# Kernel optimization log

Measured on AMD Instinct MI355X. Metric: run time of the kernel, lower is better.

The kernel has to match this reference:

```python
import jax, jax.numpy as jnp
import numpy as np

N_HEADS = 16
D_HEAD = 64  # embed_dim // n_heads = 1024 // 16


def setup_inputs() -> dict:
    key = jax.random.key(0)
    ks = jax.random.split(key, 8)
    B, S, E = 2, 2048, 1024
    return {
        "k_in": jax.random.normal(ks[0], (B, S, E), jnp.float32),
        "q_in": jax.random.normal(ks[1], (B, S, E), jnp.float32),
        "v_in": jax.random.normal(ks[2], (B, S, E), jnp.float32),
        "Wq": jax.random.normal(ks[3], (D_HEAD, D_HEAD), jnp.float32) / np.sqrt(D_HEAD),
        "Wk": jax.random.normal(ks[4], (D_HEAD, D_HEAD), jnp.float32) / np.sqrt(D_HEAD),
        "Wv": jax.random.normal(ks[5], (D_HEAD, D_HEAD), jnp.float32) / np.sqrt(D_HEAD),
        "Wo": jax.random.normal(ks[6], (E, E), jnp.float32) / np.sqrt(E),
        "bo": jnp.zeros((E,), jnp.float32),
    }


def reference(k_in, q_in, v_in, Wq, Wk, Wv, Wo, bo):
    B, Sq, E = q_in.shape
    Sk = k_in.shape[1]
    H, Dh = N_HEADS, D_HEAD
    # split heads: [B, S, H, Dh]
    q = q_in.reshape(B, Sq, H, Dh)
    k = k_in.reshape(B, Sk, H, Dh)
    v = v_in.reshape(B, Sk, H, Dh)
    # per-head linear projections (nn.Linear: x @ W.T), then [B, H, S, Dh]
    q = jnp.einsum("bshd,ed->bhse", q, Wq)
    k = jnp.einsum("bshd,ed->bhse", k, Wk)
    v = jnp.einsum("bshd,ed->bhse", v, Wv)
    # scaled dot-product attention
    scores = jnp.einsum("bhqd,bhkd->bhqk", q, k) / jnp.sqrt(jnp.asarray(Dh, q.dtype))
    attn = jax.nn.softmax(scores, axis=-1)
    ctx = jnp.einsum("bhqk,bhkd->bqhd", attn, v)  # [B, Sq, H, Dh]
    concat = ctx.reshape(B, Sq, H * Dh)
    return concat @ Wo.T + bo
```

## Files before the change

kernel.cpp:

```cpp
#include <hip/hip_runtime.h>
#include <hip/hip_fp16.h>

typedef _Float16 f16;
typedef _Float16 f16x8 __attribute__((ext_vector_type(8)));
typedef _Float16 f16x4v __attribute__((ext_vector_type(4)));
typedef float f32x4 __attribute__((ext_vector_type(4)));

#define B_ 2
#define S_ 2048
#define E_ 1024
#define H_ 16
#define DH_ 64

__device__ __forceinline__ f32x4 mfma16(f16x8 a, f16x8 b, f32x4 c) {
    return __builtin_amdgcn_mfma_f32_16x16x32_f16(a, b, c, 0, 0, 0);
}

__device__ __forceinline__ f16x8 cvt8(const float* p) {
    float4 v0 = *(const float4*)p;
    float4 v1 = *(const float4*)(p + 4);
    f16x8 r;
    r[0] = (f16)v0.x; r[1] = (f16)v0.y; r[2] = (f16)v0.z; r[3] = (f16)v0.w;
    r[4] = (f16)v1.x; r[5] = (f16)v1.y; r[6] = (f16)v1.z; r[7] = (f16)v1.w;
    return r;
}

__global__ __launch_bounds__(256) void proj_kernel(
    const float* __restrict__ q_in, const float* __restrict__ k_in,
    const float* __restrict__ v_in,
    const float* __restrict__ Wq, const float* __restrict__ Wk,
    const float* __restrict__ Wv,
    f16* __restrict__ Qg, f16* __restrict__ Kg, f16* __restrict__ Vt)
{
    int tid = threadIdx.x;
    int lane = tid & 63, wv = tid >> 6;
    int wid = blockIdx.x * 4 + wv;
    int proj = wid >> 12;
    int r = wid & 4095;
    int bh = r >> 7;
    int stile = r & 127;
    int sbase = stile * 16;
    int h = bh & 15;
    int b = bh >> 4;
    int c = lane & 15, g = lane >> 4;

    const float* x; const float* W;
    if (proj == 0)      { x = q_in; W = Wq; }
    else if (proj == 1) { x = k_in; W = Wk; }
    else                { x = v_in; W = Wv; }

    const float* xrow = x + (((size_t)(b * S_ + sbase + c) * H_ + h) << 6);
    f16x8 a0 = cvt8(xrow + g * 8);
    f16x8 a1 = cvt8(xrow + 32 + g * 8);

    f32x4 acc[4] = {};
#pragma unroll
    for (int nt = 0; nt < 4; ++nt) {
        const float* wrow = W + ((nt * 16 + c) << 6);
        f16x8 b0 = cvt8(wrow + g * 8);
        f16x8 b1 = cvt8(wrow + 32 + g * 8);
        acc[nt] = mfma16(a0, b0, acc[nt]);
        acc[nt] = mfma16(a1, b1, acc[nt]);
    }

    if (proj < 2) {
        f16* out = (proj == 0) ? Qg : Kg;
#pragma unroll
        for (int nt = 0; nt < 4; ++nt)
#pragma unroll
            for (int j = 0; j < 4; ++j) {
                int s = sbase + g * 4 + j;
                out[((size_t)bh * S_ + s) * DH_ + nt * 16 + c] = (f16)acc[nt][j];
            }
    } else {
#pragma unroll
        for (int nt = 0; nt < 4; ++nt) {
            f16x4v pk;
            pk[0] = (f16)acc[nt][0]; pk[1] = (f16)acc[nt][1];
            pk[2] = (f16)acc[nt][2]; pk[3] = (f16)acc[nt][3];
            *(f16x4v*)&Vt[((size_t)bh * DH_ + nt * 16 + c) * S_ + sbase + g * 4] = pk;
        }
    }
}

__global__ __launch_bounds__(256) void cvt_wo(const float* __restrict__ W,
                                              f16* __restrict__ out)
{
    int i = blockIdx.x * 256 + threadIdx.x;
    float4 v = *(const float4*)(W + (size_t)i * 4);
    f16x4v o;
    o[0] = (f16)v.x; o[1] = (f16)v.y; o[2] = (f16)v.z; o[3] = (f16)v.w;
    *(f16x4v*)(out + (size_t)i * 4) = o;
}

#define C1_ 0.18033688011112042f

__global__ __launch_bounds__(512, 4) void attn_kernel(
    const f16* __restrict__ Qg, const f16* __restrict__ Kg,
    const f16* __restrict__ Vt, f16* __restrict__ ctx)
{
    __shared__ __align__(16) f16 Kl[2][64 * 64];
    __shared__ __align__(16) f16 Vl[2][64 * 64];
    __shared__ __align__(16) f16 Pl[8][16 * 64];

    int tid = threadIdx.x, lane = tid & 63, wv = tid >> 6;
    int bx = blockIdx.x;
    int bh = bx >> 4, qt = bx & 15;
    int b = bh >> 4, h = bh & 15;
    int qbase = qt * 128 + wv * 16;
    int c = lane & 15, g = lane >> 4;
    int swz = (c & 7) << 3;

    const f16* Qh = Qg + (size_t)bh * S_ * DH_;
    const f16* Kh = Kg + (size_t)bh * S_ * DH_;
    const f16* Vh = Vt + (size_t)bh * DH_ * S_;

    int srow = tid >> 3, scc = tid & 7;
    int sdst = srow * 64 + ((scc * 8) ^ ((srow & 7) << 3));
    const f16* ksrc = Kh + (size_t)srow * DH_ + scc * 8;
    const f16* vsrc = Vh + (size_t)srow * S_ + scc * 8;

    f16x8 qf[2];
#pragma unroll
    for (int hh = 0; hh < 2; ++hh)
        qf[hh] = *(const f16x8*)(Qh + (size_t)(qbase + c) * DH_ + hh * 32 + g * 8);

    float m2 = -1e30f, lr = 0.f;
    f32x4 accO[4] = {};

    f16x8 kreg = *(const f16x8*)ksrc;
    f16x8 vreg = *(const f16x8*)vsrc;
    *(f16x8*)&Kl[0][sdst] = kreg;
    *(f16x8*)&Vl[0][sdst] = vreg;
    __syncthreads();

    int cur = 0;
#pragma unroll 1
    for (int kt = 0; kt < 32; ++kt) {
        if (kt < 31) {
            kreg = *(const f16x8*)(ksrc + (size_t)(kt + 1) * 64 * DH_);
            vreg = *(const f16x8*)(vsrc + (kt + 1) * 64);
        }

        const f16* KA = &Kl[cur][0];
        const f16* VA = &Vl[cur][0];

        f32x4 accS[4] = {};
#pragma unroll
        for (int ks = 0; ks < 4; ++ks) {
            f16x8 k0 = *(const f16x8*)&KA[(ks * 16 + c) * 64 + ((8 * g) ^ swz)];
            f16x8 k1 = *(const f16x8*)&KA[(ks * 16 + c) * 64 + ((32 + 8 * g) ^ swz)];
            accS[ks] = mfma16(k0, qf[0], accS[ks]);
            accS[ks] = mfma16(k1, qf[1], accS[ks]);
        }

        float rmax = fmaxf(fmaxf(accS[0][0], accS[0][1]),
                           fmaxf(accS[0][2], accS[0][3]));
#pragma unroll
        for (int ks = 1; ks < 4; ++ks)
#pragma unroll
            for (int j = 0; j < 4; ++j) rmax = fmaxf(rmax, accS[ks][j]);
        rmax = fmaxf(rmax, __shfl_xor(rmax, 16));
        rmax = fmaxf(rmax, __shfl_xor(rmax, 32));
        float pm2 = rmax * C1_;

        float al = 1.f;
        if (!__all(pm2 - m2 <= 8.f)) {
            float mn = fmaxf(m2, pm2);
            al = exp2f(m2 - mn);
            m2 = mn;
#pragma unroll
            for (int j = 0; j < 4; ++j) {
                float aj = __shfl(al, 4 * g + j);
#pragma unroll
                for (int nt = 0; nt < 4; ++nt) accO[nt][j] *= aj;
            }
        }

        float rs = 0.f;
        float p[4][4];
#pragma unroll
        for (int ks = 0; ks < 4; ++ks)
#pragma unroll
            for (int j = 0; j < 4; ++j) {
                float pv = exp2f(fmaf(accS[ks][j], C1_, -m2));
                p[ks][j] = pv; rs += pv;
            }
        rs += __shfl_xor(rs, 16);
        rs += __shfl_xor(rs, 32);
        lr = lr * al + rs;

#pragma unroll
        for (int ks = 0; ks < 4; ++ks) {
            f16x4v w;
            w[0] = (f16)p[ks][0]; w[1] = (f16)p[ks][1];
            w[2] = (f16)p[ks][2]; w[3] = (f16)p[ks][3];
            *(f16x4v*)&Pl[wv][c * 64 + ((16 * ks + 4 * g) ^ swz)] = w;
        }

#pragma unroll
        for (int kh = 0; kh < 2; ++kh) {
            f16x8 pa = *(const f16x8*)&Pl[wv][c * 64 + ((32 * kh + 8 * g) ^ swz)];
#pragma unroll
            for (int nt = 0; nt < 4; ++nt) {
                f16x8 vb = *(const f16x8*)&VA[(nt * 16 + c) * 64
                                              + ((32 * kh + 8 * g) ^ swz)];
                accO[nt] = mfma16(pa, vb, accO[nt]);
            }
        }

        if (kt < 31) {
            *(f16x8*)&Kl[cur ^ 1][sdst] = kreg;
            *(f16x8*)&Vl[cur ^ 1][sdst] = vreg;
            __syncthreads();
        }
        cur ^= 1;
    }

    float inv = 1.f / lr;
#pragma unroll
    for (int j = 0; j < 4; ++j) {
        float lj = __shfl(inv, 4 * g + j);
        int s = qbase + 4 * g + j;
#pragma unroll
        for (int nt = 0; nt < 4; ++nt)
            ctx[((size_t)b * S_ + s) * E_ + h * DH_ + nt * 16 + c] =
                (f16)(accO[nt][j] * lj);
    }
}

__global__ __launch_bounds__(256) void gemm_out(
    const f16* __restrict__ A,
    const f16* __restrict__ Bw,
    const float* __restrict__ bo,
    float* __restrict__ out)
{
    __shared__ __align__(16) f16 Al[2][128 * 64];
    __shared__ __align__(16) f16 Bl[2][64 * 64];

    int tid = threadIdx.x, lane = tid & 63, wv = tid >> 6;
    int mbase = blockIdx.x * 128, nbase = blockIdx.y * 64;
    int c = lane & 15, g = lane >> 4;
    int wr = wv >> 1, wc = wv & 1;
    int swz = (c & 7) << 3;

    int arow[4], adst[4]; const f16* asrc[4];
#pragma unroll
    for (int i = 0; i < 4; ++i) {
        int slot = tid + i * 256;
        arow[i] = slot >> 3;
        int cc = slot & 7;
        adst[i] = arow[i] * 64 + ((cc * 8) ^ ((arow[i] & 7) << 3));
        asrc[i] = A + (size_t)(mbase + arow[i]) * 1024 + cc * 8;
    }
    int bdst[2]; const f16* bsrc[2];
#pragma unroll
    for (int i = 0; i < 2; ++i) {
        int slot = tid + i * 256;
        int row = slot >> 3, cc = slot & 7;
        bdst[i] = row * 64 + ((cc * 8) ^ ((row & 7) << 3));
        bsrc[i] = Bw + (size_t)(nbase + row) * 1024 + cc * 8;
    }

    f32x4 acc[4][2] = {};

    f16x8 areg[4], breg[2];
#pragma unroll
    for (int i = 0; i < 4; ++i) areg[i] = *(const f16x8*)asrc[i];
#pragma unroll
    for (int i = 0; i < 2; ++i) breg[i] = *(const f16x8*)bsrc[i];
#pragma unroll
    for (int i = 0; i < 4; ++i) *(f16x8*)&Al[0][adst[i]] = areg[i];
#pragma unroll
    for (int i = 0; i < 2; ++i) *(f16x8*)&Bl[0][bdst[i]] = breg[i];
    __syncthreads();

    int cur = 0;
#pragma unroll 1
    for (int ks = 0; ks < 16; ++ks) {
        if (ks < 15) {
#pragma unroll
            for (int i = 0; i < 4; ++i)
                areg[i] = *(const f16x8*)(asrc[i] + (ks + 1) * 64);
#pragma unroll
            for (int i = 0; i < 2; ++i)
                breg[i] = *(const f16x8*)(bsrc[i] + (ks + 1) * 64);
        }

        const f16* AA = &Al[cur][0];
        const f16* BB = &Bl[cur][0];
#pragma unroll
        for (int kk = 0; kk < 2; ++kk) {
            f16x8 af[4], bf[2];
#pragma unroll
            for (int mi = 0; mi < 4; ++mi)
                af[mi] = *(const f16x8*)&AA[(wr * 64 + mi * 16 + c) * 64
                                            + ((32 * kk + 8 * g) ^ swz)];
#pragma unroll
            for (int ni = 0; ni < 2; ++ni)
                bf[ni] = *(const f16x8*)&BB[(wc * 32 + ni * 16 + c) * 64
                                            + ((32 * kk + 8 * g) ^ swz)];
#pragma unroll
            for (int mi = 0; mi < 4; ++mi)
#pragma unroll
                for (int ni = 0; ni < 2; ++ni)
                    acc[mi][ni] = mfma16(af[mi], bf[ni], acc[mi][ni]);
        }

        if (ks < 15) {
#pragma unroll
            for (int i = 0; i < 4; ++i) *(f16x8*)&Al[cur ^ 1][adst[i]] = areg[i];
#pragma unroll
            for (int i = 0; i < 2; ++i) *(f16x8*)&Bl[cur ^ 1][bdst[i]] = breg[i];
            __syncthreads();
        }
        cur ^= 1;
    }

#pragma unroll
    for (int ni = 0; ni < 2; ++ni) {
        float bias = bo[nbase + wc * 32 + ni * 16 + c];
#pragma unroll
        for (int mi = 0; mi < 4; ++mi)
#pragma unroll
            for (int j = 0; j < 4; ++j) {
                int m = mbase + wr * 64 + mi * 16 + g * 4 + j;
                out[(size_t)m * 1024 + nbase + wc * 32 + ni * 16 + c] =
                    acc[mi][ni][j] + bias;
            }
    }
}

extern "C" void kernel_launch(void* const* d_in, const int* in_sizes, int n_in,
                              void* d_out, int out_size, void* d_ws, size_t ws_size,
                              hipStream_t stream)
{
    const float* k_in = (const float*)d_in[0];
    const float* q_in = (const float*)d_in[1];
    const float* v_in = (const float*)d_in[2];
    const float* Wq   = (const float*)d_in[3];
    const float* Wk   = (const float*)d_in[4];
    const float* Wv   = (const float*)d_in[5];
    const float* Wo   = (const float*)d_in[6];
    const float* bo   = (const float*)d_in[7];
    float* out = (float*)d_out;

    char* ws = (char*)d_ws;
    f16* Qg  = (f16*)(ws);
    f16* Kg  = (f16*)(ws + (8u << 20));
    f16* Vt  = (f16*)(ws + (16u << 20));
    f16* ctx = (f16*)(ws + (24u << 20));
    f16* WoH = (f16*)(ws + (32u << 20));

    proj_kernel<<<dim3(3072), dim3(256), 0, stream>>>(q_in, k_in, v_in,
                                                      Wq, Wk, Wv, Qg, Kg, Vt);
    cvt_wo<<<dim3(1024), dim3(256), 0, stream>>>(Wo, WoH);
    attn_kernel<<<dim3(512), dim3(512), 0, stream>>>(Qg, Kg, Vt, ctx);
    gemm_out<<<dim3(32, 16), dim3(256), 0, stream>>>(ctx, WoH, bo, out);
}
```

Baseline: 121.1 us.

## Enlarge attention KV tiles, defer row-sum reduction, fuse Wo conversion into GEMM

The attention kernel now stages 128-key K/V tiles per barrier, which halves the number of loop iterations and syncs. Each tile is processed as two 64-key sub-steps. The row-sum shuffles are moved out of the loop, and the max reduction runs only when a rescale is needed. The separate Wo fp32-to-fp16 conversion kernel is removed, and gemm_out converts Wo on load, saving one launch at the cost of re-converting the weights in every block. s_setprio hints are also placed around the MFMA sections, and the doubled shared memory may lower occupancy.

```diff
diff --git a/kernel.cpp b/kernel.cpp
--- a/kernel.cpp
+++ b/kernel.cpp
@@ -83,24 +83,14 @@
     }
 }
 
-__global__ __launch_bounds__(256) void cvt_wo(const float* __restrict__ W,
-                                              f16* __restrict__ out)
-{
-    int i = blockIdx.x * 256 + threadIdx.x;
-    float4 v = *(const float4*)(W + (size_t)i * 4);
-    f16x4v o;
-    o[0] = (f16)v.x; o[1] = (f16)v.y; o[2] = (f16)v.z; o[3] = (f16)v.w;
-    *(f16x4v*)(out + (size_t)i * 4) = o;
-}
-
 #define C1_ 0.18033688011112042f
 
 __global__ __launch_bounds__(512, 4) void attn_kernel(
     const f16* __restrict__ Qg, const f16* __restrict__ Kg,
     const f16* __restrict__ Vt, f16* __restrict__ ctx)
 {
-    __shared__ __align__(16) f16 Kl[2][64 * 64];
-    __shared__ __align__(16) f16 Vl[2][64 * 64];
+    __shared__ __align__(16) f16 Kl[2][128 * 64];
+    __shared__ __align__(16) f16 Vl[2][64 * 128];
     __shared__ __align__(16) f16 Pl[8][16 * 64];
 
     int tid = threadIdx.x, lane = tid & 63, wv = tid >> 6;
@@ -115,10 +105,17 @@
     const f16* Kh = Kg + (size_t)bh * S_ * DH_;
     const f16* Vh = Vt + (size_t)bh * DH_ * S_;
 
-    int srow = tid >> 3, scc = tid & 7;
-    int sdst = srow * 64 + ((scc * 8) ^ ((srow & 7) << 3));
-    const f16* ksrc = Kh + (size_t)srow * DH_ + scc * 8;
-    const f16* vsrc = Vh + (size_t)srow * S_ + scc * 8;
+    int s0 = tid, s1 = tid + 512;
+    int kr0 = s0 >> 3, kc0 = s0 & 7, kr1 = s1 >> 3, kc1 = s1 & 7;
+    int kd0 = kr0 * 64 + ((kc0 * 8) ^ ((kr0 & 7) << 3));
+    int kd1 = kr1 * 64 + ((kc1 * 8) ^ ((kr1 & 7) << 3));
+    const f16* ksp0 = Kh + kr0 * 64 + kc0 * 8;
+    const f16* ksp1 = Kh + kr1 * 64 + kc1 * 8;
+    int vr0 = s0 >> 4, vc0 = s0 & 15, vr1 = s1 >> 4, vc1 = s1 & 15;
+    int vd0 = vr0 * 128 + ((vc0 * 8) ^ ((vr0 & 7) << 3));
+    int vd1 = vr1 * 128 + ((vc1 * 8) ^ ((vr1 & 7) << 3));
+    const f16* vsp0 = Vh + vr0 * S_ + vc0 * 8;
+    const f16* vsp1 = Vh + vr1 * S_ + vc1 * 8;
 
     f16x8 qf[2];
 #pragma unroll
@@ -128,95 +125,103 @@
     float m2 = -1e30f, lr = 0.f;
     f32x4 accO[4] = {};
 
-    f16x8 kreg = *(const f16x8*)ksrc;
-    f16x8 vreg = *(const f16x8*)vsrc;
-    *(f16x8*)&Kl[0][sdst] = kreg;
-    *(f16x8*)&Vl[0][sdst] = vreg;
+    f16x8 kreg0 = *(const f16x8*)ksp0, kreg1 = *(const f16x8*)ksp1;
+    f16x8 vreg0 = *(const f16x8*)vsp0, vreg1 = *(const f16x8*)vsp1;
+    *(f16x8*)&Kl[0][kd0] = kreg0; *(f16x8*)&Kl[0][kd1] = kreg1;
+    *(f16x8*)&Vl[0][vd0] = vreg0; *(f16x8*)&Vl[0][vd1] = vreg1;
     __syncthreads();
 
     int cur = 0;
 #pragma unroll 1
-    for (int kt = 0; kt < 32; ++kt) {
-        if (kt < 31) {
-            kreg = *(const f16x8*)(ksrc + (size_t)(kt + 1) * 64 * DH_);
-            vreg = *(const f16x8*)(vsrc + (kt + 1) * 64);
+    for (int kt = 0; kt < 16; ++kt) {
+        if (kt < 15) {
+            int ko = (kt + 1) * 128 * 64, vo = (kt + 1) * 128;
+            kreg0 = *(const f16x8*)(ksp0 + ko);
+            kreg1 = *(const f16x8*)(ksp1 + ko);
+            vreg0 = *(const f16x8*)(vsp0 + vo);
+            vreg1 = *(const f16x8*)(vsp1 + vo);
         }
 
         const f16* KA = &Kl[cur][0];
         const f16* VA = &Vl[cur][0];
 
-        f32x4 accS[4] = {};
-#pragma unroll
-        for (int ks = 0; ks < 4; ++ks) {
-            f16x8 k0 = *(const f16x8*)&KA[(ks * 16 + c) * 64 + ((8 * g) ^ swz)];
-            f16x8 k1 = *(const f16x8*)&KA[(ks * 16 + c) * 64 + ((32 + 8 * g) ^ swz)];
-            accS[ks] = mfma16(k0, qf[0], accS[ks]);
-            accS[ks] = mfma16(k1, qf[1], accS[ks]);
-        }
-
-        float rmax = fmaxf(fmaxf(accS[0][0], accS[0][1]),
-                           fmaxf(accS[0][2], accS[0][3]));
-#pragma unroll
-        for (int ks = 1; ks < 4; ++ks)
-#pragma unroll
-            for (int j = 0; j < 4; ++j) rmax = fmaxf(rmax, accS[ks][j]);
-        rmax = fmaxf(rmax, __shfl_xor(rmax, 16));
-        rmax = fmaxf(rmax, __shfl_xor(rmax, 32));
-        float pm2 = rmax * C1_;
-
-        float al = 1.f;
-        if (!__all(pm2 - m2 <= 8.f)) {
-            float mn = fmaxf(m2, pm2);
-            al = exp2f(m2 - mn);
-            m2 = mn;
-#pragma unroll
-            for (int j = 0; j < 4; ++j) {
-                float aj = __shfl(al, 4 * g + j);
-#pragma unroll
-                for (int nt = 0; nt < 4; ++nt) accO[nt][j] *= aj;
-            }
-        }
-
-        float rs = 0.f;
-        float p[4][4];
-#pragma unroll
-        for (int ks = 0; ks < 4; ++ks)
-#pragma unroll
-            for (int j = 0; j < 4; ++j) {
-                float pv = exp2f(fmaf(accS[ks][j], C1_, -m2));
-                p[ks][j] = pv; rs += pv;
-            }
-        rs += __shfl_xor(rs, 16);
-        rs += __shfl_xor(rs, 32);
-        lr = lr * al + rs;
-
-#pragma unroll
-        for (int ks = 0; ks < 4; ++ks) {
-            f16x4v w;
-            w[0] = (f16)p[ks][0]; w[1] = (f16)p[ks][1];
-            w[2] = (f16)p[ks][2]; w[3] = (f16)p[ks][3];
-            *(f16x4v*)&Pl[wv][c * 64 + ((16 * ks + 4 * g) ^ swz)] = w;
-        }
-
-#pragma unroll
-        for (int kh = 0; kh < 2; ++kh) {
-            f16x8 pa = *(const f16x8*)&Pl[wv][c * 64 + ((32 * kh + 8 * g) ^ swz)];
-#pragma unroll
-            for (int nt = 0; nt < 4; ++nt) {
-                f16x8 vb = *(const f16x8*)&VA[(nt * 16 + c) * 64
-                                              + ((32 * kh + 8 * g) ^ swz)];
-                accO[nt] = mfma16(pa, vb, accO[nt]);
-            }
-        }
-
-        if (kt < 31) {
-            *(f16x8*)&Kl[cur ^ 1][sdst] = kreg;
-            *(f16x8*)&Vl[cur ^ 1][sdst] = vreg;
+#pragma unroll
+        for (int st = 0; st < 2; ++st) {
+            f32x4 accS[4] = {};
+            __builtin_amdgcn_s_setprio(1);
+#pragma unroll
+            for (int ks = 0; ks < 4; ++ks) {
+                int krow = (st * 64 + ks * 16 + c) * 64;
+                f16x8 k0 = *(const f16x8*)&KA[krow + ((8 * g) ^ swz)];
+                f16x8 k1 = *(const f16x8*)&KA[krow + ((32 + 8 * g) ^ swz)];
+                accS[ks] = mfma16(k0, qf[0], accS[ks]);
+                accS[ks] = mfma16(k1, qf[1], accS[ks]);
+            }
+            __builtin_amdgcn_s_setprio(0);
+
+            float rmax = fmaxf(fmaxf(accS[0][0], accS[0][1]),
+                               fmaxf(accS[0][2], accS[0][3]));
+#pragma unroll
+            for (int ks = 1; ks < 4; ++ks)
+#pragma unroll
+                for (int j = 0; j < 4; ++j) rmax = fmaxf(rmax, accS[ks][j]);
+
+            if (!__all(fmaf(rmax, C1_, -m2) <= 8.f)) {
+                float mx = fmaxf(rmax, __shfl_xor(rmax, 16));
+                mx = fmaxf(mx, __shfl_xor(mx, 32));
+                float mn = fmaxf(m2, mx * C1_);
+                float al = exp2f(m2 - mn);
+                m2 = mn;
+                lr *= al;
+#pragma unroll
+                for (int j = 0; j < 4; ++j) {
+                    float aj = __shfl(al, 4 * g + j);
+#pragma unroll
+                    for (int nt = 0; nt < 4; ++nt) accO[nt][j] *= aj;
+                }
+            }
+
+            float p[4][4];
+#pragma unroll
+            for (int ks = 0; ks < 4; ++ks)
+#pragma unroll
+                for (int j = 0; j < 4; ++j) {
+                    float pv = exp2f(fmaf(accS[ks][j], C1_, -m2));
+                    p[ks][j] = pv; lr += pv;
+                }
+
+#pragma unroll
+            for (int ks = 0; ks < 4; ++ks) {
+                f16x4v w;
+                w[0] = (f16)p[ks][0]; w[1] = (f16)p[ks][1];
+                w[2] = (f16)p[ks][2]; w[3] = (f16)p[ks][3];
+                *(f16x4v*)&Pl[wv][c * 64 + ((16 * ks + 4 * g) ^ swz)] = w;
+            }
+
+            __builtin_amdgcn_s_setprio(1);
+#pragma unroll
+            for (int kh = 0; kh < 2; ++kh) {
+                f16x8 pa = *(const f16x8*)&Pl[wv][c * 64 + ((32 * kh + 8 * g) ^ swz)];
+#pragma unroll
+                for (int nt = 0; nt < 4; ++nt) {
+                    f16x8 vb = *(const f16x8*)&VA[(nt * 16 + c) * 128
+                                  + ((st * 64 + 32 * kh + 8 * g) ^ swz)];
+                    accO[nt] = mfma16(pa, vb, accO[nt]);
+                }
+            }
+            __builtin_amdgcn_s_setprio(0);
+        }
+
+        if (kt < 15) {
+            *(f16x8*)&Kl[cur ^ 1][kd0] = kreg0; *(f16x8*)&Kl[cur ^ 1][kd1] = kreg1;
+            *(f16x8*)&Vl[cur ^ 1][vd0] = vreg0; *(f16x8*)&Vl[cur ^ 1][vd1] = vreg1;
             __syncthreads();
         }
         cur ^= 1;
     }
 
+    lr += __shfl_xor(lr, 16);
+    lr += __shfl_xor(lr, 32);
     float inv = 1.f / lr;
 #pragma unroll
     for (int j = 0; j < 4; ++j) {
@@ -231,7 +236,7 @@
 
 __global__ __launch_bounds__(256) void gemm_out(
     const f16* __restrict__ A,
-    const f16* __restrict__ Bw,
+    const float* __restrict__ Wo,
     const float* __restrict__ bo,
     float* __restrict__ out)
 {
@@ -253,13 +258,13 @@
         adst[i] = arow[i] * 64 + ((cc * 8) ^ ((arow[i] & 7) << 3));
         asrc[i] = A + (size_t)(mbase + arow[i]) * 1024 + cc * 8;
     }
-    int bdst[2]; const f16* bsrc[2];
+    int bdst[2]; const float* bsrc[2];
 #pragma unroll
     for (int i = 0; i < 2; ++i) {
         int slot = tid + i * 256;
         int row = slot >> 3, cc = slot & 7;
         bdst[i] = row * 64 + ((cc * 8) ^ ((row & 7) << 3));
-        bsrc[i] = Bw + (size_t)(nbase + row) * 1024 + cc * 8;
+        bsrc[i] = Wo + (size_t)(nbase + row) * 1024 + cc * 8;
     }
 
     f32x4 acc[4][2] = {};
@@ -268,7 +273,7 @@
 #pragma unroll
     for (int i = 0; i < 4; ++i) areg[i] = *(const f16x8*)asrc[i];
 #pragma unroll
-    for (int i = 0; i < 2; ++i) breg[i] = *(const f16x8*)bsrc[i];
+    for (int i = 0; i < 2; ++i) breg[i] = cvt8(bsrc[i]);
 #pragma unroll
     for (int i = 0; i < 4; ++i) *(f16x8*)&Al[0][adst[i]] = areg[i];
 #pragma unroll
@@ -284,11 +289,12 @@
                 areg[i] = *(const f16x8*)(asrc[i] + (ks + 1) * 64);
 #pragma unroll
             for (int i = 0; i < 2; ++i)
-                breg[i] = *(const f16x8*)(bsrc[i] + (ks + 1) * 64);
+                breg[i] = cvt8(bsrc[i] + (ks + 1) * 64);
         }
 
         const f16* AA = &Al[cur][0];
         const f16* BB = &Bl[cur][0];
+        __builtin_amdgcn_s_setprio(1);
 #pragma unroll
         for (int kk = 0; kk < 2; ++kk) {
             f16x8 af[4], bf[2];
@@ -306,6 +312,7 @@
                 for (int ni = 0; ni < 2; ++ni)
                     acc[mi][ni] = mfma16(af[mi], bf[ni], acc[mi][ni]);
         }
+        __builtin_amdgcn_s_setprio(0);
 
         if (ks < 15) {
 #pragma unroll
@@ -350,11 +357,9 @@
     f16* Kg  = (f16*)(ws + (8u << 20));
     f16* Vt  = (f16*)(ws + (16u << 20));
     f16* ctx = (f16*)(ws + (24u << 20));
-    f16* WoH = (f16*)(ws + (32u << 20));
 
     proj_kernel<<<dim3(3072), dim3(256), 0, stream>>>(q_in, k_in, v_in,
                                                       Wq, Wk, Wv, Qg, Kg, Vt);
-    cvt_wo<<<dim3(1024), dim3(256), 0, stream>>>(Wo, WoH);
     attn_kernel<<<dim3(512), dim3(512), 0, stream>>>(Qg, Kg, Vt, ctx);
-    gemm_out<<<dim3(32, 16), dim3(256), 0, stream>>>(ctx, WoH, bo, out);
-}
+    gemm_out<<<dim3(32, 16), dim3(256), 0, stream>>>(ctx, Wo, bo, out);
+}
```

Result: no change. 119.0 us (-1.7%).
